# Performance work log

Hardware: AMD Instinct MI355X
Metric: run time of the kernel (lower is better)

The kernel has to match this reference:

```python
import jax, jax.numpy as jnp
import numpy as np

TRIANGLE_TABLE = np.array([
    [-1, -1, -1, -1, -1, -1], [1, 0, 2, -1, -1, -1], [4, 0, 3, -1, -1, -1], [1, 4, 2, 1, 3, 4],
    [3, 1, 5, -1, -1, -1], [2, 3, 0, 2, 5, 3], [1, 4, 0, 1, 5, 4], [4, 2, 5, -1, -1, -1],
    [4, 5, 2, -1, -1, -1], [4, 1, 0, 4, 5, 1], [3, 2, 0, 3, 5, 2], [1, 3, 5, -1, -1, -1],
    [4, 1, 2, 4, 3, 1], [3, 0, 4, -1, -1, -1], [2, 0, 1, -1, -1, -1], [-1, -1, -1, -1, -1, -1]], np.int32)
NUM_TRIANGLES_TABLE = np.array([0, 1, 1, 2, 1, 2, 2, 1, 1, 2, 2, 1, 2, 1, 1, 0], np.int32)
BASE_TET_EDGES = np.array([0, 1, 0, 2, 0, 3, 1, 2, 1, 3, 2, 3], np.int32)


def _make_tet_grid(R):
    # Regular grid in [0,1]^3, each cube split into 6 tets along the 0-7 diagonal.
    r1 = R + 1
    gi, gj, gk = np.meshgrid(np.arange(r1), np.arange(r1), np.arange(r1), indexing='ij')
    verts = (np.stack([gi, gj, gk], -1).reshape(-1, 3) / R).astype(np.float32)  # (Nv,3)
    ci, cj, ck = np.meshgrid(np.arange(R), np.arange(R), np.arange(R), indexing='ij')
    ci, cj, ck = ci.ravel(), cj.ravel(), ck.ravel()
    def vid(dx, dy, dz):
        return ((ci + dx) * r1 + (cj + dy)) * r1 + (ck + dz)
    corners = [vid((c >> 2) & 1, (c >> 1) & 1, c & 1) for c in range(8)]
    tet_corners = [(0, 1, 3, 7), (0, 3, 2, 7), (0, 2, 6, 7), (0, 6, 4, 7), (0, 4, 5, 7), (0, 5, 1, 7)]
    tets = np.stack([np.stack([corners[a] for a in t], -1) for t in tet_corners], 1).reshape(-1, 4)
    return verts, tets.astype(np.int32)


def setup_inputs() -> dict:
    R = 64
    verts, tets = _make_tet_grid(R)
    key = jax.random.key(0)
    k1, k2 = jax.random.split(key)
    level = jax.random.normal(k1, (verts.shape[0],), dtype=jnp.float32)
    deformation = jax.random.normal(k2, (verts.shape[0], 3), dtype=jnp.float32)
    return {
        'level': level,
        'deformation': deformation,
        'grid_vertices': jnp.asarray(verts),
        'tet_indices': jnp.asarray(tets),
        'resolution': R,
    }


def reference(level, deformation, grid_vertices, tet_indices, resolution):
    # normalize_grid_deformation: (range_hi - range_lo)/res * tanh(offsets), range = (0,1)
    pos = grid_vertices + jnp.tanh(deformation) / resolution  # (Nv,3)
    occ = level > 0                                           # (Nv,)
    occ_f = occ[tet_indices]                                  # (F,4)
    occ_sum = occ_f.sum(-1)
    valid = (occ_sum > 0) & (occ_sum < 4)
    vt = tet_indices[valid]                                   # (Fv,4)
    occ_valid = occ_f[valid]                                  # (Fv,4)
    # per-tet edges, each sorted (min,max) -> dedup
    edges = vt[:, jnp.asarray(BASE_TET_EDGES)].reshape(-1, 2)  # (6*Fv,2)
    edges = jnp.sort(edges, axis=1)
    unique_edges, idx_map = jnp.unique(edges, axis=0, return_inverse=True)
    idx_map = idx_map.reshape(-1)
    # edges that actually cross the isosurface (exactly one endpoint inside)
    mask_edges = occ[unique_edges].sum(-1) == 1               # (U,)
    mapping = jnp.where(mask_edges, jnp.cumsum(mask_edges.astype(jnp.int32)) - 1, -1)
    idx_map = mapping[idx_map].reshape(-1, 6)                 # (Fv,6)
    interp_v = unique_edges[mask_edges]                       # (M,2)
    # linear interpolation of crossing point along each edge
    ep = pos[interp_v]                                        # (M,2,3)
    es = level[interp_v] * jnp.array([1.0, -1.0], dtype=level.dtype)  # (M,2) = [sdf0, -sdf1]
    w = es[:, ::-1] / es.sum(1, keepdims=True)                # (M,2) = [-sdf1, sdf0]/(sdf0-sdf1)
    verts_out = (ep * w[:, :, None]).sum(1)                   # (M,3)
    # triangle table lookup
    v_id = jnp.array([1, 2, 4, 8], dtype=jnp.int32)
    tetindex = (occ_valid.astype(jnp.int32) * v_id).sum(-1)   # (Fv,)
    tri_tab = jnp.asarray(TRIANGLE_TABLE)
    num_tri = jnp.asarray(NUM_TRIANGLES_TABLE)[tetindex]
    m1 = num_tri == 1
    m2 = num_tri == 2
    f1 = jnp.take_along_axis(idx_map[m1], tri_tab[tetindex[m1]][:, :3], axis=1).reshape(-1, 3)
    f2 = jnp.take_along_axis(idx_map[m2], tri_tab[tetindex[m2]][:, :6], axis=1).reshape(-1, 3)
    faces = jnp.concatenate([f1, f2], axis=0)                 # (Nf,3)
    return verts_out, faces
```

## Files before the change

kernel.cpp:

```cpp
#include <hip/hip_runtime.h>
#include <math.h>


typedef unsigned long long ull;

#define ST_LD(p)    __hip_atomic_load((p), __ATOMIC_RELAXED, __HIP_MEMORY_SCOPE_AGENT)
#define ST_ST(p,v)  __hip_atomic_store((p), (v), __ATOMIC_RELAXED, __HIP_MEMORY_SCOPE_AGENT)

__device__ __constant__ int c_tri_tab[16][6] = {
    {-1,-1,-1,-1,-1,-1},{1,0,2,-1,-1,-1},{4,0,3,-1,-1,-1},{1,4,2,1,3,4},
    {3,1,5,-1,-1,-1},{2,3,0,2,5,3},{1,4,0,1,5,4},{4,2,5,-1,-1,-1},
    {4,5,2,-1,-1,-1},{4,1,0,4,5,1},{3,2,0,3,5,2},{1,3,5,-1,-1,-1},
    {4,1,2,4,3,1},{3,0,4,-1,-1,-1},{2,0,1,-1,-1,-1},{-1,-1,-1,-1,-1,-1}};
__device__ __constant__ int c_num_tri[16] = {0,1,1,2,1,2,2,1,1,2,2,1,2,1,1,0};
__device__ __constant__ int c_tc[6][4] = {{0,1,3,7},{0,3,2,7},{0,2,6,7},{0,6,4,7},{0,4,5,7},{0,5,1,7}};
__device__ __constant__ int c_te[6][6] = {
    {(0<<3)|0,(0<<3)|2,(0<<3)|6,(1<<3)|1,(1<<3)|5,(3<<3)|3},
    {(0<<3)|2,(0<<3)|1,(0<<3)|6,(2<<3)|0,(3<<3)|3,(2<<3)|4},
    {(0<<3)|1,(0<<3)|5,(0<<3)|6,(2<<3)|3,(2<<3)|4,(6<<3)|0},
    {(0<<3)|5,(0<<3)|3,(0<<3)|6,(4<<3)|1,(6<<3)|0,(4<<3)|2},
    {(0<<3)|3,(0<<3)|4,(0<<3)|6,(4<<3)|0,(4<<3)|2,(5<<3)|1},
    {(0<<3)|4,(0<<3)|0,(0<<3)|6,(1<<3)|3,(5<<3)|1,(1<<3)|5}};

#define VMASK ((1ull << 63) - 1ull)

__global__ void k_vert(const float* __restrict__ level, const float* __restrict__ deform,
                       int NV, int r1, float invR,
                       ull* __restrict__ occ64, ull* __restrict__ stateA, ull* __restrict__ prefS,
                       int* __restrict__ edgeRank, unsigned char* __restrict__ obByte,
                       uint2* __restrict__ cubeRank, int* __restrict__ totals,
                       float* __restrict__ out) {
    int b = blockIdx.x;
    int v = b * 256 + threadIdx.x;
    int R = r1 - 1, rsq = r1 * r1;
    bool valid = v < NV;
    float la = valid ? level[v] : 0.f;
    bool occv = valid && (la > 0.f);
    ull bal = __ballot(occv);
    if ((threadIdx.x & 63) == 0 && valid) occ64[v >> 6] = bal;

    int x = 0, y = 0, z = 0, flags = 0, n1 = 0, n2 = 0, cidx = 0;
    bool interior = false;
    float lb[7];
    if (valid) {
        x = v / rsq; int rem = v - x * rsq; y = rem / r1; z = rem - y * r1;
        bool bx = x < R, by = y < R, bz = z < R;
        interior = bx && by && bz;
        bool inb[7] = {bz, by, by && bz, bx, bx && bz, bx && by, interior};
        int deltas[7] = {1, r1, r1 + 1, rsq, rsq + 1, rsq + r1, rsq + r1 + 1};
        int ob = occv ? 1 : 0;
        for (int j = 0; j < 7; j++) {
            float l = inb[j] ? level[v + deltas[j]] : 0.f;
            lb[j] = l;
            bool o = inb[j] && (l > 0.f);
            ob |= (o ? 1 : 0) << (j + 1);
            if (inb[j] && (o != occv)) flags |= 1 << j;
        }
        if (interior) {
            cidx = ((x * R) + y) * R + z;
            obByte[cidx] = (unsigned char)ob;
            for (int k = 0; k < 6; k++) {
                int ti = ((ob >> c_tc[k][0]) & 1) | (((ob >> c_tc[k][1]) & 1) << 1)
                       | (((ob >> c_tc[k][2]) & 1) << 2) | (((ob >> c_tc[k][3]) & 1) << 3);
                int n = c_num_tri[ti];
                n1 += (n == 1); n2 += (n == 2);
            }
        }
    }
    int cnt = __popc(flags);
    int pk = n1 | (n2 << 16);
    int lane = threadIdx.x & 63, wv = threadIdx.x >> 6;
    int inclE = cnt, inclT = pk;
    for (int o = 1; o < 64; o <<= 1) {
        int tE = __shfl_up(inclE, o);
        int tT = __shfl_up(inclT, o);
        if (lane >= o) { inclE += tE; inclT += tT; }
    }
    __shared__ int wE[4], wT[4];
    __shared__ ull sExcl;
    if (lane == 63) { wE[wv] = inclE; wT[wv] = inclT; }
    __syncthreads();

    if (wv == 0) {
        int eb = 0, t1b = 0, t2b = 0;
        if (lane == 0) {
            eb = wE[0] + wE[1] + wE[2] + wE[3];
            int tb = wT[0] + wT[1] + wT[2] + wT[3];
            t1b = tb & 0xffff; t2b = tb >> 16;
            ST_ST(&stateA[b], (1ull << 63) | ((ull)eb << 42) | ((ull)t1b << 21) | (ull)t2b);
        }
        ull sum = 0;
        for (int w = 0; 64 * w < b; w++) {
            int i = b - 1 - 64 * w - lane;
            ull pv = (i >= 0) ? ST_LD(&prefS[i]) : 0;
            ull pm = __ballot(i >= 0 && (pv >> 63));
            int Lp = pm ? (__ffsll((long long)pm) - 1) : 64;
            ull val = 0;
            if (i >= 0 && lane < Lp) {
                ull s;
                do { s = ST_LD(&stateA[i]); } while (!(s >> 63));
                val = s & VMASK;
            } else if (i >= 0 && lane == Lp) {
                val = pv & VMASK;
            }
            for (int o = 1; o < 64; o <<= 1) val += __shfl_xor(val, o);
            sum += val;
            if (Lp < 64) break;
        }
        if (lane == 0) {
            sExcl = sum;
            ull inc = sum + (((ull)eb << 42) | ((ull)t1b << 21) | (ull)t2b);
            ST_ST(&prefS[b], (1ull << 63) | inc);
            if (b == (int)gridDim.x - 1) {
                totals[0] = (int)((inc >> 42) & 0x1FFFFF);
                totals[1] = (int)((inc >> 21) & 0x1FFFFF);
                totals[2] = (int)(inc & 0x1FFFFF);
            }
        }
    }
    __syncthreads();

    ull ex = sExcl;
    int exclE = (int)((ex >> 42) & 0x1FFFFF);
    int excl1 = (int)((ex >> 21) & 0x1FFFFF);
    int excl2 = (int)(ex & 0x1FFFFF);
    int woffE = 0, woffT = 0;
    for (int w = 0; w < wv; w++) { woffE += wE[w]; woffT += wT[w]; }
    int rank0 = exclE + woffE + inclE - cnt;
    int tExcl = woffT + inclT - pk;
    if (interior)
        cubeRank[cidx] = make_uint2((unsigned)(excl1 + (tExcl & 0xffff)),
                                    (unsigned)(excl2 + (tExcl >> 16)));

    if (valid) {
        int er[7]; int r = rank0;
        for (int j = 0; j < 7; j++) er[j] = ((flags >> j) & 1) ? r++ : -1;
        for (int j = 0; j < 7; j++) edgeRank[(size_t)j * NV + v] = er[j];
    }
    if (flags) {
        int deltas[7] = {1, r1, r1 + 1, rsq, rsq + 1, rsq + r1, rsq + r1 + 1};
        const int dxs[7] = {0, 0, 0, 1, 1, 1, 1};
        const int dys[7] = {0, 1, 1, 0, 0, 1, 1};
        const int dzs[7] = {1, 0, 1, 0, 1, 0, 1};
        float pax = x * invR + tanhf(deform[3 * v])     * invR;
        float pay = y * invR + tanhf(deform[3 * v + 1]) * invR;
        float paz = z * invR + tanhf(deform[3 * v + 2]) * invR;
        int r = rank0;
        for (int j = 0; j < 7; j++) {
            if (!((flags >> j) & 1)) continue;
            int bb = v + deltas[j];
            float lbv = lb[j];
            float denom = la - lbv;
            float w0 = (-lbv) / denom;
            float w1f = la / denom;
            float pbx = (x + dxs[j]) * invR + tanhf(deform[3 * bb])     * invR;
            float pby = (y + dys[j]) * invR + tanhf(deform[3 * bb + 1]) * invR;
            float pbz = (z + dzs[j]) * invR + tanhf(deform[3 * bb + 2]) * invR;
            out[3 * r]     = pax * w0 + pbx * w1f;
            out[3 * r + 1] = pay * w0 + pby * w1f;
            out[3 * r + 2] = paz * w0 + pbz * w1f;
            r++;
        }
    }
}

__global__ void k_face(int NV, int r1, int NT,
                       const unsigned char* __restrict__ obByte,
                       const uint2* __restrict__ cubeRank,
                       const int* __restrict__ edgeRank, const int* __restrict__ totals,
                       float* __restrict__ out) {
    __shared__ ull tab[256];
    if (threadIdx.x < 256) {
        int ob = threadIdx.x;
        ull w = 0;
        for (int k = 0; k < 6; k++) {
            int ti = ((ob >> c_tc[k][0]) & 1) | (((ob >> c_tc[k][1]) & 1) << 1)
                   | (((ob >> c_tc[k][2]) & 1) << 2) | (((ob >> c_tc[k][3]) & 1) << 3);
            w |= (ull)ti << (4 * k);
            w |= (ull)c_num_tri[ti] << (32 + 2 * k);
        }
        tab[ob] = w;
    }
    __syncthreads();

    int t = blockIdx.x * 256 + threadIdx.x;
    if (t >= NT) return;
    int c = t / 6;
    int k = t - c * 6;
    int ob = obByte[c];
    ull w = tab[ob];
    int nt = (int)(w >> (32 + 2 * k)) & 3;
    if (nt == 0) return;
    int ti = (int)(w >> (4 * k)) & 15;
    int pre1 = 0, pre2 = 0;
    for (int kk = 0; kk < k; kk++) {
        int m = (int)(w >> (32 + 2 * kk)) & 3;
        pre1 += (m == 1); pre2 += (m == 2);
    }
    uint2 cr = cubeRank[c];
    int R = r1 - 1, rsq = r1 * r1;
    int rr = R * R;
    int cx = c / rr; int rem = c - cx * rr; int cy = rem / R; int cz = rem - cy * R;
    int v = (cx * r1 + cy) * r1 + cz;

    int M = totals[0], N1 = totals[1];
    float* faces = out + 3 * (size_t)M;
    int off[8] = {0, 1, r1, r1 + 1, rsq, rsq + 1, rsq + r1, rsq + r1 + 1};
    int ne = nt * 3;
    float vals[6];
    for (int e = 0; e < ne; e++) {
        int le = c_tri_tab[ti][e];
        int ce = c_te[k][le];
        int a = v + off[ce >> 3];
        vals[e] = (float)edgeRank[(size_t)(ce & 7) * NV + a];
    }
    if (nt == 1) {
        size_t base = 3 * (size_t)(cr.x + pre1);
        faces[base] = vals[0]; faces[base + 1] = vals[1]; faces[base + 2] = vals[2];
    } else {
        size_t base = 3 * ((size_t)N1 + 2 * (size_t)(cr.y + pre2));
        for (int e = 0; e < 6; e++) faces[base + e] = vals[e];
    }
}

extern "C" void kernel_launch(void* const* d_in, const int* in_sizes, int n_in,
                              void* d_out, int out_size, void* d_ws, size_t ws_size,
                              hipStream_t stream) {
    const float* level  = (const float*)d_in[0];
    const float* deform = (const float*)d_in[1];
    int NV = in_sizes[0];
    int r1 = 1;
    while ((long long)r1 * r1 * r1 < (long long)NV) r1++;
    int R = r1 - 1;
    float invR = 1.0f / (float)R;

    int nb = (NV + 255) / 256;
    int nw = (NV + 63) / 64;
    int NC = R * R * R;
    int NT = 6 * NC;
    int nbT = (NT + 255) / 256;

    char* w = (char*)d_ws;
    int* edgeRank = (int*)w;
    w += (((size_t)NV * 7 * sizeof(int)) + 255) & ~(size_t)255;
    ull* occ64 = (ull*)w;
    w += (((size_t)nw * 8) + 255) & ~(size_t)255;
    unsigned char* obByte = (unsigned char*)w;
    w += (((size_t)NC) + 255) & ~(size_t)255;
    uint2* cubeRank = (uint2*)w;
    w += (((size_t)NC * 8) + 255) & ~(size_t)255;
    ull* stateA = (ull*)w;
    ull* prefS = stateA + nb;
    int* totals = (int*)(prefS + nb);
    size_t zbytes = (size_t)nb * 16 + 4 * sizeof(int);

    float* out = (float*)d_out;

    hipMemsetAsync(stateA, 0, zbytes, stream);
    k_vert<<<nb, 256, 0, stream>>>(level, deform, NV, r1, invR, occ64, stateA, prefS,
                                   edgeRank, obByte, cubeRank, totals, out);
    k_face<<<nbT, 256, 0, stream>>>(NV, r1, NT, obByte, cubeRank, edgeRank, totals, out);
}
```

Before: 136.9 us.

## Fuse vertex and face kernels into one cooperative kernel with grid sync

Merges the vertex/edge pass and the face pass into a single cooperative kernel. The decoupled look-back scan is replaced by a grid.sync, after which every block sums all per-block totals itself. A second grid.sync separates edge-rank production from face emission. Faces are now emitted one cube per thread, looping over its six tets instead of one thread per tet. This removes the memset, a second kernel launch and the spin-waiting look-back, at the cost of two grid-wide barriers, a requirement that all blocks be co-resident, and less parallelism in the face phase.

Result: slower. 440.5 us (+221.8%).

```diff
diff --git a/kernel.cpp b/kernel.cpp
--- a/kernel.cpp
+++ b/kernel.cpp
@@ -1,11 +1,10 @@
 #include <hip/hip_runtime.h>
+#include <hip/hip_cooperative_groups.h>
 #include <math.h>
 
-
+namespace cg = cooperative_groups;
 typedef unsigned long long ull;
 
-#define ST_LD(p)    __hip_atomic_load((p), __ATOMIC_RELAXED, __HIP_MEMORY_SCOPE_AGENT)
-#define ST_ST(p,v)  __hip_atomic_store((p), (v), __ATOMIC_RELAXED, __HIP_MEMORY_SCOPE_AGENT)
 
 __device__ __constant__ int c_tri_tab[16][6] = {
     {-1,-1,-1,-1,-1,-1},{1,0,2,-1,-1,-1},{4,0,3,-1,-1,-1},{1,4,2,1,3,4},
@@ -22,156 +21,127 @@
     {(0<<3)|3,(0<<3)|4,(0<<3)|6,(4<<3)|0,(4<<3)|2,(5<<3)|1},
     {(0<<3)|4,(0<<3)|0,(0<<3)|6,(1<<3)|3,(5<<3)|1,(1<<3)|5}};
 
-#define VMASK ((1ull << 63) - 1ull)
-
-__global__ void k_vert(const float* __restrict__ level, const float* __restrict__ deform,
-                       int NV, int r1, float invR,
-                       ull* __restrict__ occ64, ull* __restrict__ stateA, ull* __restrict__ prefS,
-                       int* __restrict__ edgeRank, unsigned char* __restrict__ obByte,
-                       uint2* __restrict__ cubeRank, int* __restrict__ totals,
-                       float* __restrict__ out) {
+__global__ __launch_bounds__(256, 6)
+void k_mt(const float* __restrict__ level, const float* __restrict__ deform,
+          int NV, int r1, float invR,
+          ull* __restrict__ stateA, int* __restrict__ edgeRank,
+          unsigned char* __restrict__ obByte, uint2* __restrict__ cubeRank,
+          int NC, float* __restrict__ out) {
+    cg::grid_group grid = cg::this_grid();
     int b = blockIdx.x;
-    int v = b * 256 + threadIdx.x;
+    int tid = threadIdx.x;
+    int nb = (int)gridDim.x;
+    int v = b * 256 + tid;
     int R = r1 - 1, rsq = r1 * r1;
+    int lane = tid & 63, wv = tid >> 6;
+
+    __shared__ int wE[4], wT[4];
+    __shared__ ull rB[4], rA[4];
+    __shared__ ull tab[256];
+
     bool valid = v < NV;
-    float la = valid ? level[v] : 0.f;
-    bool occv = valid && (la > 0.f);
-    ull bal = __ballot(occv);
-    if ((threadIdx.x & 63) == 0 && valid) occ64[v >> 6] = bal;
-
-    int x = 0, y = 0, z = 0, flags = 0, n1 = 0, n2 = 0, cidx = 0;
-    bool interior = false;
-    float lb[7];
+    int flags = 0, pk = 0;
     if (valid) {
-        x = v / rsq; int rem = v - x * rsq; y = rem / r1; z = rem - y * r1;
+        int x = v / rsq; int rem = v - x * rsq; int y = rem / r1; int z = rem - y * r1;
         bool bx = x < R, by = y < R, bz = z < R;
-        interior = bx && by && bz;
-        bool inb[7] = {bz, by, by && bz, bx, bx && bz, bx && by, interior};
+        bool inb[7] = {bz, by, by && bz, bx, bx && bz, bx && by, bx && by && bz};
         int deltas[7] = {1, r1, r1 + 1, rsq, rsq + 1, rsq + r1, rsq + r1 + 1};
+        bool occv = level[v] > 0.f;
         int ob = occv ? 1 : 0;
         for (int j = 0; j < 7; j++) {
-            float l = inb[j] ? level[v + deltas[j]] : 0.f;
-            lb[j] = l;
-            bool o = inb[j] && (l > 0.f);
+            bool o = inb[j] && (level[v + deltas[j]] > 0.f);
             ob |= (o ? 1 : 0) << (j + 1);
             if (inb[j] && (o != occv)) flags |= 1 << j;
         }
-        if (interior) {
-            cidx = ((x * R) + y) * R + z;
-            obByte[cidx] = (unsigned char)ob;
+        if (inb[6]) {
+            int n1 = 0, n2 = 0;
             for (int k = 0; k < 6; k++) {
                 int ti = ((ob >> c_tc[k][0]) & 1) | (((ob >> c_tc[k][1]) & 1) << 1)
                        | (((ob >> c_tc[k][2]) & 1) << 2) | (((ob >> c_tc[k][3]) & 1) << 3);
                 int n = c_num_tri[ti];
                 n1 += (n == 1); n2 += (n == 2);
             }
+            pk = n1 | (n2 << 16);
+            obByte[((x * R) + y) * R + z] = (unsigned char)ob;
         }
     }
     int cnt = __popc(flags);
-    int pk = n1 | (n2 << 16);
-    int lane = threadIdx.x & 63, wv = threadIdx.x >> 6;
     int inclE = cnt, inclT = pk;
     for (int o = 1; o < 64; o <<= 1) {
         int tE = __shfl_up(inclE, o);
         int tT = __shfl_up(inclT, o);
         if (lane >= o) { inclE += tE; inclT += tT; }
     }
-    __shared__ int wE[4], wT[4];
-    __shared__ ull sExcl;
     if (lane == 63) { wE[wv] = inclE; wT[wv] = inclT; }
     __syncthreads();
-
-    if (wv == 0) {
-        int eb = 0, t1b = 0, t2b = 0;
-        if (lane == 0) {
-            eb = wE[0] + wE[1] + wE[2] + wE[3];
-            int tb = wT[0] + wT[1] + wT[2] + wT[3];
-            t1b = tb & 0xffff; t2b = tb >> 16;
-            ST_ST(&stateA[b], (1ull << 63) | ((ull)eb << 42) | ((ull)t1b << 21) | (ull)t2b);
-        }
-        ull sum = 0;
-        for (int w = 0; 64 * w < b; w++) {
-            int i = b - 1 - 64 * w - lane;
-            ull pv = (i >= 0) ? ST_LD(&prefS[i]) : 0;
-            ull pm = __ballot(i >= 0 && (pv >> 63));
-            int Lp = pm ? (__ffsll((long long)pm) - 1) : 64;
-            ull val = 0;
-            if (i >= 0 && lane < Lp) {
-                ull s;
-                do { s = ST_LD(&stateA[i]); } while (!(s >> 63));
-                val = s & VMASK;
-            } else if (i >= 0 && lane == Lp) {
-                val = pv & VMASK;
-            }
-            for (int o = 1; o < 64; o <<= 1) val += __shfl_xor(val, o);
-            sum += val;
-            if (Lp < 64) break;
-        }
-        if (lane == 0) {
-            sExcl = sum;
-            ull inc = sum + (((ull)eb << 42) | ((ull)t1b << 21) | (ull)t2b);
-            ST_ST(&prefS[b], (1ull << 63) | inc);
-            if (b == (int)gridDim.x - 1) {
-                totals[0] = (int)((inc >> 42) & 0x1FFFFF);
-                totals[1] = (int)((inc >> 21) & 0x1FFFFF);
-                totals[2] = (int)(inc & 0x1FFFFF);
-            }
-        }
-    }
+    if (tid == 0) {
+        int eb = wE[0] + wE[1] + wE[2] + wE[3];
+        int tb = wT[0] + wT[1] + wT[2] + wT[3];
+        stateA[b] = ((ull)eb << 42) | ((ull)(tb & 0xffff) << 21) | (ull)(tb >> 16);
+    }
+    grid.sync();
+
+    ull sB = 0, sA = 0;
+    for (int i = tid; i < nb; i += 256) {
+        ull s = stateA[i];
+        sA += s;
+        if (i < b) sB += s;
+    }
+    for (int o = 1; o < 64; o <<= 1) { sB += __shfl_xor(sB, o); sA += __shfl_xor(sA, o); }
+    if (lane == 0) { rB[wv] = sB; rA[wv] = sA; }
     __syncthreads();
-
-    ull ex = sExcl;
-    int exclE = (int)((ex >> 42) & 0x1FFFFF);
-    int excl1 = (int)((ex >> 21) & 0x1FFFFF);
-    int excl2 = (int)(ex & 0x1FFFFF);
+    ull exP  = rB[0] + rB[1] + rB[2] + rB[3];
+    ull allP = rA[0] + rA[1] + rA[2] + rA[3];
+    int exclE = (int)((exP >> 42) & 0x1FFFFF);
+    int excl1 = (int)((exP >> 21) & 0x1FFFFF);
+    int excl2 = (int)(exP & 0x1FFFFF);
+    int M  = (int)((allP >> 42) & 0x1FFFFF);
+    int N1 = (int)((allP >> 21) & 0x1FFFFF);
+
     int woffE = 0, woffT = 0;
     for (int w = 0; w < wv; w++) { woffE += wE[w]; woffT += wT[w]; }
     int rank0 = exclE + woffE + inclE - cnt;
     int tExcl = woffT + inclT - pk;
-    if (interior)
-        cubeRank[cidx] = make_uint2((unsigned)(excl1 + (tExcl & 0xffff)),
-                                    (unsigned)(excl2 + (tExcl >> 16)));
 
     if (valid) {
+        int x = v / rsq; int rem = v - x * rsq; int y = rem / r1; int z = rem - y * r1;
+        if (x < R && y < R && z < R)
+            cubeRank[((x * R) + y) * R + z] =
+                make_uint2((unsigned)(excl1 + (tExcl & 0xffff)),
+                           (unsigned)(excl2 + (tExcl >> 16)));
         int er[7]; int r = rank0;
         for (int j = 0; j < 7; j++) er[j] = ((flags >> j) & 1) ? r++ : -1;
         for (int j = 0; j < 7; j++) edgeRank[(size_t)j * NV + v] = er[j];
-    }
-    if (flags) {
-        int deltas[7] = {1, r1, r1 + 1, rsq, rsq + 1, rsq + r1, rsq + r1 + 1};
-        const int dxs[7] = {0, 0, 0, 1, 1, 1, 1};
-        const int dys[7] = {0, 1, 1, 0, 0, 1, 1};
-        const int dzs[7] = {1, 0, 1, 0, 1, 0, 1};
-        float pax = x * invR + tanhf(deform[3 * v])     * invR;
-        float pay = y * invR + tanhf(deform[3 * v + 1]) * invR;
-        float paz = z * invR + tanhf(deform[3 * v + 2]) * invR;
-        int r = rank0;
-        for (int j = 0; j < 7; j++) {
-            if (!((flags >> j) & 1)) continue;
-            int bb = v + deltas[j];
-            float lbv = lb[j];
-            float denom = la - lbv;
-            float w0 = (-lbv) / denom;
-            float w1f = la / denom;
-            float pbx = (x + dxs[j]) * invR + tanhf(deform[3 * bb])     * invR;
-            float pby = (y + dys[j]) * invR + tanhf(deform[3 * bb + 1]) * invR;
-            float pbz = (z + dzs[j]) * invR + tanhf(deform[3 * bb + 2]) * invR;
-            out[3 * r]     = pax * w0 + pbx * w1f;
-            out[3 * r + 1] = pay * w0 + pby * w1f;
-            out[3 * r + 2] = paz * w0 + pbz * w1f;
-            r++;
-        }
-    }
-}
-
-__global__ void k_face(int NV, int r1, int NT,
-                       const unsigned char* __restrict__ obByte,
-                       const uint2* __restrict__ cubeRank,
-                       const int* __restrict__ edgeRank, const int* __restrict__ totals,
-                       float* __restrict__ out) {
-    __shared__ ull tab[256];
-    if (threadIdx.x < 256) {
-        int ob = threadIdx.x;
+        if (flags) {
+            int deltas[7] = {1, r1, r1 + 1, rsq, rsq + 1, rsq + r1, rsq + r1 + 1};
+            const int dxs[7] = {0, 0, 0, 1, 1, 1, 1};
+            const int dys[7] = {0, 1, 1, 0, 0, 1, 1};
+            const int dzs[7] = {1, 0, 1, 0, 1, 0, 1};
+            float la = level[v];
+            float pax = x * invR + tanhf(deform[3 * v])     * invR;
+            float pay = y * invR + tanhf(deform[3 * v + 1]) * invR;
+            float paz = z * invR + tanhf(deform[3 * v + 2]) * invR;
+            r = rank0;
+            for (int j = 0; j < 7; j++) {
+                if (!((flags >> j) & 1)) continue;
+                int bb = v + deltas[j];
+                float lbv = level[bb];
+                float denom = la - lbv;
+                float w0 = (-lbv) / denom;
+                float w1f = la / denom;
+                float pbx = (x + dxs[j]) * invR + tanhf(deform[3 * bb])     * invR;
+                float pby = (y + dys[j]) * invR + tanhf(deform[3 * bb + 1]) * invR;
+                float pbz = (z + dzs[j]) * invR + tanhf(deform[3 * bb + 2]) * invR;
+                out[3 * r]     = pax * w0 + pbx * w1f;
+                out[3 * r + 1] = pay * w0 + pby * w1f;
+                out[3 * r + 2] = paz * w0 + pbz * w1f;
+                r++;
+            }
+        }
+    }
+
+    {
+        int ob = tid;
         ull w = 0;
         for (int k = 0; k < 6; k++) {
             int ti = ((ob >> c_tc[k][0]) & 1) | (((ob >> c_tc[k][1]) & 1) << 1)
@@ -181,45 +151,42 @@
         }
         tab[ob] = w;
     }
-    __syncthreads();
-
-    int t = blockIdx.x * 256 + threadIdx.x;
-    if (t >= NT) return;
-    int c = t / 6;
-    int k = t - c * 6;
-    int ob = obByte[c];
-    ull w = tab[ob];
-    int nt = (int)(w >> (32 + 2 * k)) & 3;
-    if (nt == 0) return;
-    int ti = (int)(w >> (4 * k)) & 15;
-    int pre1 = 0, pre2 = 0;
-    for (int kk = 0; kk < k; kk++) {
-        int m = (int)(w >> (32 + 2 * kk)) & 3;
-        pre1 += (m == 1); pre2 += (m == 2);
-    }
-    uint2 cr = cubeRank[c];
-    int R = r1 - 1, rsq = r1 * r1;
+    __threadfence();
+    grid.sync();
+
+    float* faces = out + 3 * (size_t)M;
     int rr = R * R;
-    int cx = c / rr; int rem = c - cx * rr; int cy = rem / R; int cz = rem - cy * R;
-    int v = (cx * r1 + cy) * r1 + cz;
-
-    int M = totals[0], N1 = totals[1];
-    float* faces = out + 3 * (size_t)M;
     int off[8] = {0, 1, r1, r1 + 1, rsq, rsq + 1, rsq + r1, rsq + r1 + 1};
-    int ne = nt * 3;
-    float vals[6];
-    for (int e = 0; e < ne; e++) {
-        int le = c_tri_tab[ti][e];
-        int ce = c_te[k][le];
-        int a = v + off[ce >> 3];
-        vals[e] = (float)edgeRank[(size_t)(ce & 7) * NV + a];
-    }
-    if (nt == 1) {
-        size_t base = 3 * (size_t)(cr.x + pre1);
-        faces[base] = vals[0]; faces[base + 1] = vals[1]; faces[base + 2] = vals[2];
-    } else {
-        size_t base = 3 * ((size_t)N1 + 2 * (size_t)(cr.y + pre2));
-        for (int e = 0; e < 6; e++) faces[base + e] = vals[e];
+    for (int c = b * 256 + tid; c < NC; c += nb * 256) {
+        int ob = obByte[c];
+        ull w = tab[ob];
+        if (!(w >> 32)) continue;
+        uint2 cr = cubeRank[c];
+        int cx = c / rr; int rem = c - cx * rr; int cy = rem / R; int cz = rem - cy * R;
+        int vb = (cx * r1 + cy) * r1 + cz;
+        int rk1 = (int)cr.x, rk2 = (int)cr.y;
+        for (int k = 0; k < 6; k++) {
+            int nt = (int)(w >> (32 + 2 * k)) & 3;
+            if (nt == 0) continue;
+            int ti = (int)(w >> (4 * k)) & 15;
+            float vals[6];
+            int ne = nt * 3;
+            for (int e = 0; e < ne; e++) {
+                int le = c_tri_tab[ti][e];
+                int ce = c_te[k][le];
+                int a = vb + off[ce >> 3];
+                vals[e] = (float)edgeRank[(size_t)(ce & 7) * NV + a];
+            }
+            if (nt == 1) {
+                size_t base = 3 * (size_t)rk1;
+                faces[base] = vals[0]; faces[base + 1] = vals[1]; faces[base + 2] = vals[2];
+                rk1++;
+            } else {
+                size_t base = 3 * ((size_t)N1 + 2 * (size_t)rk2);
+                for (int e = 0; e < 6; e++) faces[base + e] = vals[e];
+                rk2++;
+            }
+        }
     }
 }
 
@@ -235,29 +202,21 @@
     float invR = 1.0f / (float)R;
 
     int nb = (NV + 255) / 256;
-    int nw = (NV + 63) / 64;
     int NC = R * R * R;
-    int NT = 6 * NC;
-    int nbT = (NT + 255) / 256;
 
     char* w = (char*)d_ws;
     int* edgeRank = (int*)w;
     w += (((size_t)NV * 7 * sizeof(int)) + 255) & ~(size_t)255;
-    ull* occ64 = (ull*)w;
-    w += (((size_t)nw * 8) + 255) & ~(size_t)255;
     unsigned char* obByte = (unsigned char*)w;
     w += (((size_t)NC) + 255) & ~(size_t)255;
     uint2* cubeRank = (uint2*)w;
     w += (((size_t)NC * 8) + 255) & ~(size_t)255;
     ull* stateA = (ull*)w;
-    ull* prefS = stateA + nb;
-    int* totals = (int*)(prefS + nb);
-    size_t zbytes = (size_t)nb * 16 + 4 * sizeof(int);
 
     float* out = (float*)d_out;
 
-    hipMemsetAsync(stateA, 0, zbytes, stream);
-    k_vert<<<nb, 256, 0, stream>>>(level, deform, NV, r1, invR, occ64, stateA, prefS,
-                                   edgeRank, obByte, cubeRank, totals, out);
-    k_face<<<nbT, 256, 0, stream>>>(NV, r1, NT, obByte, cubeRank, edgeRank, totals, out);
+    void* args[] = {(void*)&level, (void*)&deform, (void*)&NV, (void*)&r1, (void*)&invR,
+                    (void*)&stateA, (void*)&edgeRank, (void*)&obByte, (void*)&cubeRank,
+                    (void*)&NC, (void*)&out};
+    hipLaunchCooperativeKernel((void*)k_mt, dim3(nb), dim3(256), args, 0, stream);
 }
```
